# Performance work log

Hardware: AMD Instinct MI355X
Metric: run time of the kernel (lower is better)

Reference implementation:

```python
import jax, jax.numpy as jnp
import numpy as np

B, D, E, T, H = 16384, 1024, 8, 4, 512


def setup_inputs() -> dict:
    key = jax.random.key(0)
    ks = jax.random.split(key, 7)
    s_e = 1.0 / np.sqrt(D)
    s_t = 1.0 / np.sqrt(H)
    return {
        "x": jax.random.normal(ks[0], (B, D), dtype=jnp.float32),
        "We": jax.random.uniform(ks[1], (E, D, H), minval=-s_e, maxval=s_e, dtype=jnp.float32),
        "be": jax.random.uniform(ks[2], (E, H), minval=-s_e, maxval=s_e, dtype=jnp.float32),
        "Wg": jax.random.uniform(ks[3], (T, D, E), minval=-s_e, maxval=s_e, dtype=jnp.float32),
        "bg": jax.random.uniform(ks[4], (T, E), minval=-s_e, maxval=s_e, dtype=jnp.float32),
        "Wt": jax.random.uniform(ks[5], (T, H, 1), minval=-s_t, maxval=s_t, dtype=jnp.float32),
        "bt": jax.random.uniform(ks[6], (T, 1), minval=-s_t, maxval=s_t, dtype=jnp.float32),
    }


def reference(x, We, be, Wg, bg, Wt, bt):
    # Experts: [B, E, H] -- batched GEMM over all experts at once
    expert_out = jnp.einsum("bd,edh->beh", x, We) + be[None, :, :]
    # Gates per task: logits [B, T, E], softmax over experts
    gate_logits = jnp.einsum("bd,tde->bte", x, Wg) + bg[None, :, :]
    gate_w = jax.nn.softmax(gate_logits, axis=-1)
    # Weighted sum of expert outputs per task: [B, T, H]
    mixed = jnp.einsum("bte,beh->bth", gate_w, expert_out)
    # Task heads: [B, T, 1]
    task_out = jnp.einsum("bth,tho->bto", mixed, Wt) + bt[None, :, :]
    # Match original: list of T tensors [B, 1] -> stacked [T, B, 1]
    return jnp.transpose(task_out, (1, 0, 2))
```

## Files before the change

kernel.cpp:

```cpp
#include <hip/hip_runtime.h>
#include <math.h>


typedef float  f32x4  __attribute__((ext_vector_type(4)));
typedef short  bf16x8 __attribute__((ext_vector_type(8)));

#define WFRAG_OFF_BYTES 262272

__device__ __forceinline__ void cvt_pair(float f0, float f1, unsigned int& hi, unsigned int& lo) {
  unsigned int u0 = __float_as_uint(f0), u1 = __float_as_uint(f1);
  unsigned int r0 = u0 + 0x7FFFu + ((u0 >> 16) & 1u);
  unsigned int r1 = u1 + 0x7FFFu + ((u1 >> 16) & 1u);
  float h0 = __uint_as_float(r0 & 0xFFFF0000u);
  float h1 = __uint_as_float(r1 & 0xFFFF0000u);
  hi = (r0 >> 16) | (r1 & 0xFFFF0000u);
  float l0 = f0 - h0, l1 = f1 - h1;
  unsigned int s0 = __float_as_uint(l0), s1 = __float_as_uint(l1);
  unsigned int q0 = s0 + 0x7FFFu + ((s0 >> 16) & 1u);
  unsigned int q1 = s1 + 0x7FFFu + ((s1 >> 16) & 1u);
  lo = (q0 >> 16) | (q1 & 0xFFFF0000u);
}

__device__ __forceinline__ unsigned int cvtpk_bf16(float a, float b) {
  unsigned int r;
  asm("v_cvt_pk_bf16_f32 %0, %1, %2" : "=v"(r) : "v"(a), "v"(b));
  return r;
}
__device__ __forceinline__ void cvt_pair_fast(float f0, float f1, unsigned int& hi, unsigned int& lo) {
  unsigned int h = cvtpk_bf16(f0, f1);
  float h0 = __uint_as_float(h << 16);
  float h1 = __uint_as_float(h & 0xFFFF0000u);
  lo = cvtpk_bf16(f0 - h0, f1 - h1);
  hi = h;
}

__global__ __launch_bounds__(256) void mmoe_precompute(
    const float* __restrict__ We, const float* __restrict__ be,
    const float* __restrict__ Wg, const float* __restrict__ Wt,
    float* __restrict__ ws)
{
  float* Wcomb = ws;
  float* cbias = ws + 65536;
  const int tid = threadIdx.x, lane = tid & 63, w = tid >> 6;
  const int pairid = blockIdx.x * 4 + w;
  const int e = pairid >> 10, d = pairid & 1023;

  const float* werow = We + (size_t)pairid * 512;
  float a0 = 0.f, a1 = 0.f, a2 = 0.f, a3 = 0.f;
#pragma unroll
  for (int j = 0; j < 8; ++j) {
    int h = lane + j * 64;
    float wv = werow[h];
    a0 = fmaf(wv, Wt[h],        a0);
    a1 = fmaf(wv, Wt[512 + h],  a1);
    a2 = fmaf(wv, Wt[1024 + h], a2);
    a3 = fmaf(wv, Wt[1536 + h], a3);
  }
#pragma unroll
  for (int m = 1; m < 64; m <<= 1) {
    a0 += __shfl_xor(a0, m, 64); a1 += __shfl_xor(a1, m, 64);
    a2 += __shfl_xor(a2, m, 64); a3 += __shfl_xor(a3, m, 64);
  }
  if (lane == 0) {
    Wcomb[d * 64 + 32 + 0 * 8 + e] = a0;
    Wcomb[d * 64 + 32 + 1 * 8 + e] = a1;
    Wcomb[d * 64 + 32 + 2 * 8 + e] = a2;
    Wcomb[d * 64 + 32 + 3 * 8 + e] = a3;
  }
  if (e == 0 && lane < 32) {
    int t = lane >> 3, ee = lane & 7;
    Wcomb[d * 64 + t * 8 + ee] = Wg[t * 8192 + d * 8 + ee];
  }
  if (d == 0) {
    float b0 = 0.f, b1 = 0.f, b2 = 0.f, b3 = 0.f;
#pragma unroll
    for (int j = 0; j < 8; ++j) {
      int h = lane + j * 64;
      float bv = be[e * 512 + h];
      b0 = fmaf(bv, Wt[h],        b0);
      b1 = fmaf(bv, Wt[512 + h],  b1);
      b2 = fmaf(bv, Wt[1024 + h], b2);
      b3 = fmaf(bv, Wt[1536 + h], b3);
    }
#pragma unroll
    for (int m = 1; m < 64; m <<= 1) {
      b0 += __shfl_xor(b0, m, 64); b1 += __shfl_xor(b1, m, 64);
      b2 += __shfl_xor(b2, m, 64); b3 += __shfl_xor(b3, m, 64);
    }
    if (lane == 0) {
      cbias[0 * 8 + e] = b0; cbias[1 * 8 + e] = b1;
      cbias[2 * 8 + e] = b2; cbias[3 * 8 + e] = b3;
    }
  }
}

__global__ __launch_bounds__(256) void mmoe_swizzle(const float* __restrict__ Wc,
                                                    uint4* __restrict__ wf)
{
  const int idx = blockIdx.x * 256 + threadIdx.x;
  const int ks = idx >> 9;
  const int rem = idx & 511;
  const int vn = rem >> 6, l = rem & 63;
  const int v = vn >> 2, nf = vn & 3;
  const int n = nf * 16 + (l & 15);
  const int kbase = ks * 32 + (l >> 4) * 8;
  unsigned int pk[4];
#pragma unroll
  for (int p = 0; p < 4; ++p) {
    float f0 = Wc[(size_t)(kbase + 2 * p) * 64 + n];
    float f1 = Wc[(size_t)(kbase + 2 * p + 1) * 64 + n];
    unsigned int hi, lo;
    cvt_pair(f0, f1, hi, lo);
    pk[p] = v ? lo : hi;
  }
  uint4 val; val.x = pk[0]; val.y = pk[1]; val.z = pk[2]; val.w = pk[3];
  wf[idx] = val;
}

union UC { unsigned int u[4]; bf16x8 v; };

template <int S>
__device__ __forceinline__ void mmoe_step(
    const float4* __restrict__ xp0, const float4* __restrict__ xp1,
    const bf16x8* __restrict__ bptr, int l,
    float4 (&xbuf)[4][2][2], bf16x8 (&breg)[2][8], f32x4 (&acc)[2][4])
{
  constexpr int D = S & 3;
  constexpr int P = S & 1;
  float4 xa0 = xbuf[D][0][0], xa1 = xbuf[D][0][1];
  float4 xb0 = xbuf[D][1][0], xb1 = xbuf[D][1][1];
  if constexpr (S + 4 < 32) {
    xbuf[D][0][0] = xp0[(S + 4) * 8];
    xbuf[D][0][1] = xp0[(S + 4) * 8 + 1];
    xbuf[D][1][0] = xp1[(S + 4) * 8];
    xbuf[D][1][1] = xp1[(S + 4) * 8 + 1];
  }
  UC A0h, A0l, A1h, A1l;
  cvt_pair_fast(xa0.x, xa0.y, A0h.u[0], A0l.u[0]);
  cvt_pair_fast(xa0.z, xa0.w, A0h.u[1], A0l.u[1]);
  cvt_pair_fast(xa1.x, xa1.y, A0h.u[2], A0l.u[2]);
  cvt_pair_fast(xa1.z, xa1.w, A0h.u[3], A0l.u[3]);
  cvt_pair_fast(xb0.x, xb0.y, A1h.u[0], A1l.u[0]);
  cvt_pair_fast(xb0.z, xb0.w, A1h.u[1], A1l.u[1]);
  cvt_pair_fast(xb1.x, xb1.y, A1h.u[2], A1l.u[2]);
  cvt_pair_fast(xb1.z, xb1.w, A1h.u[3], A1l.u[3]);

#pragma unroll
  for (int j = 0; j < 4; ++j) {
    acc[0][j] = __builtin_amdgcn_mfma_f32_16x16x32_bf16(A0h.v, breg[P][j], acc[0][j], 0, 0, 0);
  }
#pragma unroll
  for (int j = 0; j < 4; ++j) {
    acc[1][j] = __builtin_amdgcn_mfma_f32_16x16x32_bf16(A1h.v, breg[P][j], acc[1][j], 0, 0, 0);
  }
#pragma unroll
  for (int j = 0; j < 4; ++j) {
    acc[0][j] = __builtin_amdgcn_mfma_f32_16x16x32_bf16(A0h.v, breg[P][j + 4], acc[0][j], 0, 0, 0);
  }
#pragma unroll
  for (int j = 0; j < 4; ++j) {
    acc[1][j] = __builtin_amdgcn_mfma_f32_16x16x32_bf16(A1h.v, breg[P][j + 4], acc[1][j], 0, 0, 0);
  }
#pragma unroll
  for (int j = 0; j < 4; ++j) {
    acc[0][j] = __builtin_amdgcn_mfma_f32_16x16x32_bf16(A0l.v, breg[P][j], acc[0][j], 0, 0, 0);
  }
#pragma unroll
  for (int j = 0; j < 4; ++j) {
    acc[1][j] = __builtin_amdgcn_mfma_f32_16x16x32_bf16(A1l.v, breg[P][j], acc[1][j], 0, 0, 0);
  }
  if constexpr (S + 2 < 32) {
#pragma unroll
    for (int vn = 0; vn < 8; ++vn)
      breg[P][vn] = bptr[(S + 2) * 512 + vn * 64 + l];
  }
}

__global__ __launch_bounds__(64, 1) void mmoe_main(
    const float* __restrict__ x,
    const float* __restrict__ bgp,
    const float* __restrict__ btp,
    const float* __restrict__ ws,
    float* __restrict__ out)
{
  __shared__ float cmat[2048];
  const int l   = threadIdx.x;
  const int b0g = blockIdx.x * 32;
  const float* cbias = ws + 65536;
  const bf16x8* __restrict__ bptr =
      (const bf16x8*)((const unsigned char*)ws + WFRAG_OFF_BYTES);

  const float4* __restrict__ xp0 =
      (const float4*)(x + (size_t)(b0g + (l & 15)) * 1024) + (l >> 4) * 2;
  const float4* __restrict__ xp1 = xp0 + 16 * 256;

  float4 xbuf[4][2][2];
  bf16x8 breg[2][8];
  f32x4  acc[2][4];
#pragma unroll
  for (int f = 0; f < 2; ++f)
#pragma unroll
    for (int nf = 0; nf < 4; ++nf) acc[f][nf] = (f32x4){0.f, 0.f, 0.f, 0.f};

#pragma unroll
  for (int p = 0; p < 4; ++p) {
    xbuf[p][0][0] = xp0[p * 8]; xbuf[p][0][1] = xp0[p * 8 + 1];
    xbuf[p][1][0] = xp1[p * 8]; xbuf[p][1][1] = xp1[p * 8 + 1];
  }
#pragma unroll
  for (int vn = 0; vn < 8; ++vn) breg[0][vn] = bptr[vn * 64 + l];
#pragma unroll
  for (int vn = 0; vn < 8; ++vn) breg[1][vn] = bptr[512 + vn * 64 + l];

#define MSTEP(S) mmoe_step<S>(xp0, xp1, bptr, l, xbuf, breg, acc);
  MSTEP(0)  MSTEP(1)  MSTEP(2)  MSTEP(3)  MSTEP(4)  MSTEP(5)  MSTEP(6)  MSTEP(7)
  MSTEP(8)  MSTEP(9)  MSTEP(10) MSTEP(11) MSTEP(12) MSTEP(13) MSTEP(14) MSTEP(15)
  MSTEP(16) MSTEP(17) MSTEP(18) MSTEP(19) MSTEP(20) MSTEP(21) MSTEP(22) MSTEP(23)
  MSTEP(24) MSTEP(25) MSTEP(26) MSTEP(27) MSTEP(28) MSTEP(29) MSTEP(30) MSTEP(31)
#undef MSTEP

#pragma unroll
  for (int f = 0; f < 2; ++f)
#pragma unroll
    for (int nf = 0; nf < 4; ++nf)
#pragma unroll
      for (int r = 0; r < 4; ++r)
        cmat[(f * 16 + (l >> 4) * 4 + r) * 64 + nf * 16 + (l & 15)] = acc[f][nf][r];
  __syncthreads();

#pragma unroll
  for (int p = 0; p < 2; ++p) {
    const int idx = p * 64 + l;
    const int row = idx >> 2, t = idx & 3;
    const float4 ga = *(const float4*)&cmat[row * 64 + t * 8];
    const float4 gb = *(const float4*)&cmat[row * 64 + t * 8 + 4];
    const float4 sa = *(const float4*)&cmat[row * 64 + 32 + t * 8];
    const float4 sb = *(const float4*)&cmat[row * 64 + 32 + t * 8 + 4];
    float g[8] = {ga.x, ga.y, ga.z, ga.w, gb.x, gb.y, gb.z, gb.w};
    float s[8] = {sa.x, sa.y, sa.z, sa.w, sb.x, sb.y, sb.z, sb.w};
#pragma unroll
    for (int e = 0; e < 8; ++e) {
      g[e] += bgp[t * 8 + e];
      s[e] += cbias[t * 8 + e];
    }
    float m = g[0];
#pragma unroll
    for (int e = 1; e < 8; ++e) m = fmaxf(m, g[e]);
    float Z = 0.f, num = 0.f;
#pragma unroll
    for (int e = 0; e < 8; ++e) {
      float p2 = __expf(g[e] - m);
      Z += p2;
      num = fmaf(p2, s[e], num);
    }
    out[t * 16384 + b0g + row] = num / Z + btp[t];
  }
}

extern "C" void kernel_launch(void* const* d_in, const int* in_sizes, int n_in,
                              void* d_out, int out_size, void* d_ws, size_t ws_size,
                              hipStream_t stream) {
  const float* x  = (const float*)d_in[0];
  const float* We = (const float*)d_in[1];
  const float* be = (const float*)d_in[2];
  const float* Wg = (const float*)d_in[3];
  const float* bg = (const float*)d_in[4];
  const float* Wt = (const float*)d_in[5];
  const float* bt = (const float*)d_in[6];
  float* out = (float*)d_out;
  float* ws  = (float*)d_ws;

  uint4* wf = (uint4*)((unsigned char*)d_ws + WFRAG_OFF_BYTES);

  hipLaunchKernelGGL(mmoe_precompute, dim3(2048), dim3(256), 0, stream, We, be, Wg, Wt, ws);
  hipLaunchKernelGGL(mmoe_swizzle,    dim3(64),   dim3(256), 0, stream, ws, wf);
  hipLaunchKernelGGL(mmoe_main,       dim3(512),  dim3(64),  0, stream, x, bg, bt, ws, out);
}
```

Baseline: 142.5 us.

## Split the K dimension across four waves per block with an LDS reduction

The main kernel goes from one wave per block walking all of K=1024 to four waves per block, each handling a quarter of K (8 steps instead of 32). Each wave writes its partial 32x64 accumulator tile to its own slice of shared memory, and the first 128 threads sum the four partials before the softmax and mix epilogue. The goal is to shorten the serial MFMA and load chain per block and raise the number of waves per CU, since 512 single-wave blocks left the GPU underoccupied. The cost is four times the LDS footprint plus the extra reduction pass, and the prefetch pipeline now fills and drains within only 8 steps.

```diff
diff --git a/kernel.cpp b/kernel.cpp
--- a/kernel.cpp
+++ b/kernel.cpp
@@ -122,14 +122,14 @@
 template <int S>
 __device__ __forceinline__ void mmoe_step(
     const float4* __restrict__ xp0, const float4* __restrict__ xp1,
-    const bf16x8* __restrict__ bptr, int l,
+    const bf16x8* __restrict__ bptrw, int l,
     float4 (&xbuf)[4][2][2], bf16x8 (&breg)[2][8], f32x4 (&acc)[2][4])
 {
   constexpr int D = S & 3;
   constexpr int P = S & 1;
   float4 xa0 = xbuf[D][0][0], xa1 = xbuf[D][0][1];
   float4 xb0 = xbuf[D][1][0], xb1 = xbuf[D][1][1];
-  if constexpr (S + 4 < 32) {
+  if constexpr (S + 4 < 8) {
     xbuf[D][0][0] = xp0[(S + 4) * 8];
     xbuf[D][0][1] = xp0[(S + 4) * 8 + 1];
     xbuf[D][1][0] = xp1[(S + 4) * 8];
@@ -146,52 +146,48 @@
   cvt_pair_fast(xb1.z, xb1.w, A1h.u[3], A1l.u[3]);
 
 #pragma unroll
-  for (int j = 0; j < 4; ++j) {
+  for (int j = 0; j < 4; ++j)
     acc[0][j] = __builtin_amdgcn_mfma_f32_16x16x32_bf16(A0h.v, breg[P][j], acc[0][j], 0, 0, 0);
-  }
-#pragma unroll
-  for (int j = 0; j < 4; ++j) {
+#pragma unroll
+  for (int j = 0; j < 4; ++j)
     acc[1][j] = __builtin_amdgcn_mfma_f32_16x16x32_bf16(A1h.v, breg[P][j], acc[1][j], 0, 0, 0);
-  }
-#pragma unroll
-  for (int j = 0; j < 4; ++j) {
+#pragma unroll
+  for (int j = 0; j < 4; ++j)
     acc[0][j] = __builtin_amdgcn_mfma_f32_16x16x32_bf16(A0h.v, breg[P][j + 4], acc[0][j], 0, 0, 0);
-  }
-#pragma unroll
-  for (int j = 0; j < 4; ++j) {
+#pragma unroll
+  for (int j = 0; j < 4; ++j)
     acc[1][j] = __builtin_amdgcn_mfma_f32_16x16x32_bf16(A1h.v, breg[P][j + 4], acc[1][j], 0, 0, 0);
-  }
-#pragma unroll
-  for (int j = 0; j < 4; ++j) {
+#pragma unroll
+  for (int j = 0; j < 4; ++j)
     acc[0][j] = __builtin_amdgcn_mfma_f32_16x16x32_bf16(A0l.v, breg[P][j], acc[0][j], 0, 0, 0);
-  }
-#pragma unroll
-  for (int j = 0; j < 4; ++j) {
+#pragma unroll
+  for (int j = 0; j < 4; ++j)
     acc[1][j] = __builtin_amdgcn_mfma_f32_16x16x32_bf16(A1l.v, breg[P][j], acc[1][j], 0, 0, 0);
-  }
-  if constexpr (S + 2 < 32) {
+  if constexpr (S + 2 < 8) {
 #pragma unroll
     for (int vn = 0; vn < 8; ++vn)
-      breg[P][vn] = bptr[(S + 2) * 512 + vn * 64 + l];
-  }
-}
-
-__global__ __launch_bounds__(64, 1) void mmoe_main(
+      breg[P][vn] = bptrw[(S + 2) * 512 + vn * 64 + l];
+  }
+}
+
+__global__ __launch_bounds__(256, 2) void mmoe_main(
     const float* __restrict__ x,
     const float* __restrict__ bgp,
     const float* __restrict__ btp,
     const float* __restrict__ ws,
     float* __restrict__ out)
 {
-  __shared__ float cmat[2048];
-  const int l   = threadIdx.x;
+  __shared__ float cmat[4 * 2048];
+  const int tid = threadIdx.x;
+  const int l   = tid & 63;
+  const int w   = tid >> 6;
   const int b0g = blockIdx.x * 32;
   const float* cbias = ws + 65536;
-  const bf16x8* __restrict__ bptr =
-      (const bf16x8*)((const unsigned char*)ws + WFRAG_OFF_BYTES);
+  const bf16x8* __restrict__ bptrw =
+      (const bf16x8*)((const unsigned char*)ws + WFRAG_OFF_BYTES) + w * 8 * 512;
 
   const float4* __restrict__ xp0 =
-      (const float4*)(x + (size_t)(b0g + (l & 15)) * 1024) + (l >> 4) * 2;
+      (const float4*)(x + (size_t)(b0g + (l & 15)) * 1024) + w * 64 + (l >> 4) * 2;
   const float4* __restrict__ xp1 = xp0 + 16 * 256;
 
   float4 xbuf[4][2][2];
@@ -208,16 +204,18 @@
     xbuf[p][1][0] = xp1[p * 8]; xbuf[p][1][1] = xp1[p * 8 + 1];
   }
 #pragma unroll
-  for (int vn = 0; vn < 8; ++vn) breg[0][vn] = bptr[vn * 64 + l];
-#pragma unroll
-  for (int vn = 0; vn < 8; ++vn) breg[1][vn] = bptr[512 + vn * 64 + l];
-
-#define MSTEP(S) mmoe_step<S>(xp0, xp1, bptr, l, xbuf, breg, acc);
-  MSTEP(0)  MSTEP(1)  MSTEP(2)  MSTEP(3)  MSTEP(4)  MSTEP(5)  MSTEP(6)  MSTEP(7)
-  MSTEP(8)  MSTEP(9)  MSTEP(10) MSTEP(11) MSTEP(12) MSTEP(13) MSTEP(14) MSTEP(15)
-  MSTEP(16) MSTEP(17) MSTEP(18) MSTEP(19) MSTEP(20) MSTEP(21) MSTEP(22) MSTEP(23)
-  MSTEP(24) MSTEP(25) MSTEP(26) MSTEP(27) MSTEP(28) MSTEP(29) MSTEP(30) MSTEP(31)
-#undef MSTEP
+  for (int vn = 0; vn < 8; ++vn) breg[0][vn] = bptrw[vn * 64 + l];
+#pragma unroll
+  for (int vn = 0; vn < 8; ++vn) breg[1][vn] = bptrw[512 + vn * 64 + l];
+
+  mmoe_step<0>(xp0, xp1, bptrw, l, xbuf, breg, acc);
+  mmoe_step<1>(xp0, xp1, bptrw, l, xbuf, breg, acc);
+  mmoe_step<2>(xp0, xp1, bptrw, l, xbuf, breg, acc);
+  mmoe_step<3>(xp0, xp1, bptrw, l, xbuf, breg, acc);
+  mmoe_step<4>(xp0, xp1, bptrw, l, xbuf, breg, acc);
+  mmoe_step<5>(xp0, xp1, bptrw, l, xbuf, breg, acc);
+  mmoe_step<6>(xp0, xp1, bptrw, l, xbuf, breg, acc);
+  mmoe_step<7>(xp0, xp1, bptrw, l, xbuf, breg, acc);
 
 #pragma unroll
   for (int f = 0; f < 2; ++f)
@@ -225,19 +223,24 @@
     for (int nf = 0; nf < 4; ++nf)
 #pragma unroll
       for (int r = 0; r < 4; ++r)
-        cmat[(f * 16 + (l >> 4) * 4 + r) * 64 + nf * 16 + (l & 15)] = acc[f][nf][r];
+        cmat[w * 2048 + (f * 16 + (l >> 4) * 4 + r) * 64 + nf * 16 + (l & 15)] = acc[f][nf][r];
   __syncthreads();
 
-#pragma unroll
-  for (int p = 0; p < 2; ++p) {
-    const int idx = p * 64 + l;
-    const int row = idx >> 2, t = idx & 3;
-    const float4 ga = *(const float4*)&cmat[row * 64 + t * 8];
-    const float4 gb = *(const float4*)&cmat[row * 64 + t * 8 + 4];
-    const float4 sa = *(const float4*)&cmat[row * 64 + 32 + t * 8];
-    const float4 sb = *(const float4*)&cmat[row * 64 + 32 + t * 8 + 4];
-    float g[8] = {ga.x, ga.y, ga.z, ga.w, gb.x, gb.y, gb.z, gb.w};
-    float s[8] = {sa.x, sa.y, sa.z, sa.w, sb.x, sb.y, sb.z, sb.w};
+  if (tid < 128) {
+    const int row = tid >> 2, t = tid & 3;
+    float g[8] = {0.f, 0.f, 0.f, 0.f, 0.f, 0.f, 0.f, 0.f};
+    float s[8] = {0.f, 0.f, 0.f, 0.f, 0.f, 0.f, 0.f, 0.f};
+#pragma unroll
+    for (int wv = 0; wv < 4; ++wv) {
+      const float4 ga = *(const float4*)&cmat[wv * 2048 + row * 64 + t * 8];
+      const float4 gb = *(const float4*)&cmat[wv * 2048 + row * 64 + t * 8 + 4];
+      const float4 sa = *(const float4*)&cmat[wv * 2048 + row * 64 + 32 + t * 8];
+      const float4 sb = *(const float4*)&cmat[wv * 2048 + row * 64 + 32 + t * 8 + 4];
+      g[0] += ga.x; g[1] += ga.y; g[2] += ga.z; g[3] += ga.w;
+      g[4] += gb.x; g[5] += gb.y; g[6] += gb.z; g[7] += gb.w;
+      s[0] += sa.x; s[1] += sa.y; s[2] += sa.z; s[3] += sa.w;
+      s[4] += sb.x; s[5] += sb.y; s[6] += sb.z; s[7] += sb.w;
+    }
 #pragma unroll
     for (int e = 0; e < 8; ++e) {
       g[e] += bgp[t * 8 + e];
@@ -274,5 +277,5 @@
 
   hipLaunchKernelGGL(mmoe_precompute, dim3(2048), dim3(256), 0, stream, We, be, Wg, Wt, ws);
   hipLaunchKernelGGL(mmoe_swizzle,    dim3(64),   dim3(256), 0, stream, ws, wf);
-  hipLaunchKernelGGL(mmoe_main,       dim3(512),  dim3(64),  0, stream, x, bg, bt, ws, out);
-}
+  hipLaunchKernelGGL(mmoe_main,       dim3(512),  dim3(256), 0, stream, x, bg, bt, ws, out);
+}
```

Measured after the change: 124.3 us. -12.7%, faster.
